# Kernel tuning notes

Hardware: AMD Instinct MI355X
Metric: run time of the kernel (lower is better)

Reference implementation:

```python
import jax, jax.numpy as jnp
import numpy as np

N = 100000
E = 1600000
D_IN = 128
D_OUT = 128


def setup_inputs() -> dict:
    key = jax.random.key(0)
    ks = jax.random.split(key, 6)
    seq = jax.random.normal(ks[0], (N, D_IN), dtype=jnp.float32)
    edge_src = jax.random.randint(ks[1], (E,), 0, N, dtype=jnp.int32)
    edge_dst = jax.random.randint(ks[2], (E,), 0, N, dtype=jnp.int32)
    adj_vals = jax.random.uniform(ks[3], (E,), dtype=jnp.float32)
    # xavier_uniform for [out, in] -> stored as [in, out] for x @ W
    lim = float(np.sqrt(6.0 / (D_IN + D_OUT)))
    w_fc = jax.random.uniform(ks[4], (D_IN, D_OUT), jnp.float32, -lim, lim)
    w_proj = jax.random.uniform(ks[5], (D_IN, D_OUT), jnp.float32, -lim, lim)
    b_proj = jnp.zeros((D_OUT,), jnp.float32)
    bias = jnp.zeros((D_OUT,), jnp.float32)
    return {"seq": seq, "edge_src": edge_src, "edge_dst": edge_dst,
            "adj_vals": adj_vals, "w_fc": w_fc, "w_proj": w_proj,
            "b_proj": b_proj, "bias": bias}


def reference(seq, edge_src, edge_dst, adj_vals, w_fc, w_proj, b_proj, bias):
    # h = fc(seq)  (no bias)
    h = seq @ w_fc                                  # [N, D_OUT]
    # spmm(adj, h): out[i] = sum_{e: dst=i} vals[e] * h[src[e]]
    msgs = adj_vals[:, None] * h[edge_src]          # [E, D_OUT]
    agg = jax.ops.segment_sum(msgs, edge_dst, num_segments=N)
    # bias add + residual proj(seq) add + tanh
    out = jnp.tanh(agg + bias + seq @ w_proj + b_proj)
    return out
```

## Files before the change

kernel.cpp:

```cpp
#include <hip/hip_runtime.h>
#include <math.h>


typedef __attribute__((ext_vector_type(8))) short short8;
typedef __attribute__((ext_vector_type(4))) float float4v;
typedef __attribute__((ext_vector_type(2))) _Float16 half2v;

#define PG 128
#define NBMAX 2048

static __device__ __forceinline__ short f2bf(float x) {
    unsigned u = __float_as_uint(x);
    unsigned r = (u + 0x7fffu + ((u >> 16) & 1u)) >> 16;
    return (short)r;
}
static __device__ __forceinline__ float bf2f(short h) {
    return __uint_as_float(((unsigned)(unsigned short)h) << 16);
}

__global__ __launch_bounds__(256)
void wconv_kernel(const float* __restrict__ w, short* __restrict__ whi,
                  short* __restrict__ wlo) {
    const int i = blockIdx.x * 256 + threadIdx.x;
    const float4 v = ((const float4*)w)[i];
    const int k = i >> 5;
    const int c4 = (i & 31) * 4;
    float xs[4] = {v.x, v.y, v.z, v.w};
    #pragma unroll
    for (int j = 0; j < 4; j++) {
        const short hi = f2bf(xs[j]);
        const short lo = f2bf(xs[j] - bf2f(hi));
        whi[(c4 + j) * 128 + k] = hi;
        wlo[(c4 + j) * 128 + k] = lo;
    }
}

#define KP 136

__global__ __launch_bounds__(256, 2)
void mm_mfma_kernel(const float* __restrict__ seq, const short* __restrict__ whi,
                    const short* __restrict__ wlo,
                    const float* __restrict__ b0p, const float* __restrict__ b1p,
                    float* __restrict__ out, _Float16* __restrict__ out16,
                    int N, int add_bias) {
    __shared__ short wt_hi[128 * KP];
    __shared__ short wt_lo[128 * KP];

    const int tid = threadIdx.x;
    for (int i = tid; i < 2048; i += 256) {
        const int row = i >> 4;
        const int k8  = (i & 15) * 8;
        *(float4*)&wt_hi[row * KP + k8] = ((const float4*)whi)[i];
        *(float4*)&wt_lo[row * KP + k8] = ((const float4*)wlo)[i];
    }
    __syncthreads();

    const int wave = tid >> 6;
    const int lane = tid & 63;
    const int q = lane >> 4;
    const int c = lane & 15;
    const int R = blockIdx.x * 64 + wave * 16;
    const int rowL = (R + c < N) ? (R + c) : (N - 1);

    float4v acc[8];
    #pragma unroll
    for (int ct = 0; ct < 8; ct++) acc[ct] = (float4v){0.f, 0.f, 0.f, 0.f};

    #pragma unroll
    for (int t = 0; t < 4; t++) {
        const int kk = t * 32 + q * 8;
        const float4 a0 = *(const float4*)&seq[(size_t)rowL * 128 + kk];
        const float4 a1 = *(const float4*)&seq[(size_t)rowL * 128 + kk + 4];
        float xs[8] = {a0.x, a0.y, a0.z, a0.w, a1.x, a1.y, a1.z, a1.w};
        union { short s[8]; short8 v; } ahi, alo;
        #pragma unroll
        for (int j = 0; j < 8; j++) {
            const short hi = f2bf(xs[j]);
            ahi.s[j] = hi;
            alo.s[j] = f2bf(xs[j] - bf2f(hi));
        }
        #pragma unroll
        for (int ct = 0; ct < 8; ct++) {
            const int n = ct * 16 + c;
            const short8 bhi = *(const short8*)&wt_hi[n * KP + kk];
            const short8 blo = *(const short8*)&wt_lo[n * KP + kk];
            acc[ct] = __builtin_amdgcn_mfma_f32_16x16x32_bf16(ahi.v, bhi, acc[ct], 0, 0, 0);
            acc[ct] = __builtin_amdgcn_mfma_f32_16x16x32_bf16(ahi.v, blo, acc[ct], 0, 0, 0);
            acc[ct] = __builtin_amdgcn_mfma_f32_16x16x32_bf16(alo.v, bhi, acc[ct], 0, 0, 0);
        }
    }

    if (out16) {
        #pragma unroll
        for (int ct = 0; ct < 8; ct++) {
            const int col = ct * 16 + c;
            #pragma unroll
            for (int r = 0; r < 4; r++) {
                const int row = R + q * 4 + r;
                if (row < N) out16[(size_t)row * 128 + col] = (_Float16)acc[ct][r];
            }
        }
    } else {
        #pragma unroll
        for (int ct = 0; ct < 8; ct++) {
            const int col = ct * 16 + c;
            float badd = 0.f;
            if (add_bias) badd = b0p[col] + b1p[col];
            #pragma unroll
            for (int r = 0; r < 4; r++) {
                const int row = R + q * 4 + r;
                if (row < N) out[(size_t)row * 128 + col] = acc[ct][r] + badd;
            }
        }
    }
}


__global__ __launch_bounds__(256)
void phist_kernel(const int* __restrict__ edst, int* __restrict__ hcnt,
                  int E, int S, int NB) {
    __shared__ int cnt[NBMAX];
    const int g = blockIdx.x;
    const int tid = threadIdx.x;
    for (int b = tid; b < NB; b += 256) cnt[b] = 0;
    __syncthreads();
    const int lo = g * S;
    const int hi = (lo + S < E) ? (lo + S) : E;
    for (int i = lo + tid; i < hi; i += 256)
        atomicAdd(&cnt[edst[i] >> 6], 1);
    __syncthreads();
    for (int b = tid; b < NB; b += 256) hcnt[b * PG + g] = cnt[b];
}

__global__ __launch_bounds__(256)
void pscan1_kernel(const int* __restrict__ in, int* __restrict__ out,
                   int* __restrict__ bsum, int L) {
    __shared__ int s[256];
    const int t = threadIdx.x;
    const int base = blockIdx.x * 1024 + t * 4;
    int v0 = (base + 0 < L) ? in[base + 0] : 0;
    int v1 = (base + 1 < L) ? in[base + 1] : 0;
    int v2 = (base + 2 < L) ? in[base + 2] : 0;
    int v3 = (base + 3 < L) ? in[base + 3] : 0;
    const int mysum = v0 + v1 + v2 + v3;
    s[t] = mysum;
    __syncthreads();
    for (int o = 1; o < 256; o <<= 1) {
        int add = (t >= o) ? s[t - o] : 0;
        __syncthreads();
        s[t] += add;
        __syncthreads();
    }
    const int excl = s[t] - mysum;
    if (base + 0 < L) out[base + 0] = excl;
    if (base + 1 < L) out[base + 1] = excl + v0;
    if (base + 2 < L) out[base + 2] = excl + v0 + v1;
    if (base + 3 < L) out[base + 3] = excl + v0 + v1 + v2;
    if (t == 255) bsum[blockIdx.x] = s[255];
}

__global__ __launch_bounds__(256)
void pscan2_kernel(const int* __restrict__ bsum, int* __restrict__ ebsum, int nb) {
    __shared__ int s[256];
    const int t = threadIdx.x;
    const int v = (t < nb) ? bsum[t] : 0;
    s[t] = v;
    __syncthreads();
    for (int o = 1; o < 256; o <<= 1) {
        int add = (t >= o) ? s[t - o] : 0;
        __syncthreads();
        s[t] += add;
        __syncthreads();
    }
    if (t < nb) ebsum[t] = s[t] - v;
}

__global__ __launch_bounds__(256)
void paddback_kernel(int* __restrict__ pos, const int* __restrict__ ebsum,
                     int* __restrict__ bstart, int L, int NB, int E) {
    const int add = ebsum[blockIdx.x];
    const int base = blockIdx.x * 1024 + threadIdx.x * 4;
    #pragma unroll
    for (int j = 0; j < 4; j++) {
        const int idx = base + j;
        if (idx < L) {
            const int v = pos[idx] + add;
            pos[idx] = v;
            if ((idx & (PG - 1)) == 0) bstart[idx / PG] = v;
        }
    }
    if (blockIdx.x == 0 && threadIdx.x == 0) bstart[NB] = E;
}

__global__ __launch_bounds__(256)
void pscatter_kernel(const int* __restrict__ esrc, const int* __restrict__ edst,
                     const float* __restrict__ vals, const int* __restrict__ pos,
                     int2* __restrict__ sedge, int E, int S, int NB) {
    __shared__ int cur[NBMAX];
    const int g = blockIdx.x;
    const int tid = threadIdx.x;
    for (int b = tid; b < NB; b += 256) cur[b] = pos[b * PG + g];
    __syncthreads();
    const int lo = g * S;
    const int hi = (lo + S < E) ? (lo + S) : E;
    for (int i = lo + tid; i < hi; i += 256) {
        const int d = edst[i];
        const int p = atomicAdd(&cur[d >> 6], 1);
        sedge[p] = make_int2((esrc[i] << 6) | (d & 63), __float_as_int(vals[i]));
    }
}

#define CAP 2048

__global__ __launch_bounds__(256, 8)
void aggregate_sorted(const int* __restrict__ bstart, const int2* __restrict__ sedge,
                      const _Float16* __restrict__ h, float* __restrict__ out, int N) {
    __shared__ int2 ebuf[CAP];
    __shared__ int cnt[64], sc[64], off[65], cur[64];
    const int b = blockIdx.x;
    const int tid = threadIdx.x;
    const int beg = bstart[b];
    const int total = bstart[b + 1] - beg;
    const int cl = total < CAP ? total : CAP;

    if (tid < 64) cnt[tid] = 0;
    __syncthreads();
    for (int i = tid; i < cl; i += 256)
        atomicAdd(&cnt[sedge[beg + i].x & 63], 1);
    __syncthreads();
    if (tid < 64) sc[tid] = cnt[tid];
    __syncthreads();
    for (int o = 1; o < 64; o <<= 1) {
        int add = (tid < 64 && tid >= o) ? sc[tid - o] : 0;
        __syncthreads();
        if (tid < 64) sc[tid] += add;
        __syncthreads();
    }
    if (tid < 64) { off[tid] = sc[tid] - cnt[tid]; cur[tid] = sc[tid] - cnt[tid]; }
    if (tid == 63) off[64] = sc[63];
    __syncthreads();
    for (int i = tid; i < cl; i += 256) {
        const int2 e = sedge[beg + i];
        const int p = atomicAdd(&cur[e.x & 63], 1);
        ebuf[p] = e;
    }
    __syncthreads();

    const int wave = tid >> 6;
    const int lane = tid & 63;
    const half2v* hp = (const half2v*)h;

    for (int n = wave * 16; n < wave * 16 + 16; n++) {
        const int node = b * 64 + n;
        if (node >= N) break;
        float2 acc = make_float2(0.f, 0.f);
        const int e0 = off[n], e1 = off[n + 1];
        int j = e0;
        for (; j + 4 <= e1; j += 4) {
            const int2 ea = ebuf[j], eb = ebuf[j + 1], ec = ebuf[j + 2], ed = ebuf[j + 3];
            const half2v h0 = hp[(size_t)(ea.x >> 6) * 64 + lane];
            const half2v h1 = hp[(size_t)(eb.x >> 6) * 64 + lane];
            const half2v h2 = hp[(size_t)(ec.x >> 6) * 64 + lane];
            const half2v h3 = hp[(size_t)(ed.x >> 6) * 64 + lane];
            const float v0 = __int_as_float(ea.y), v1 = __int_as_float(eb.y);
            const float v2 = __int_as_float(ec.y), v3 = __int_as_float(ed.y);
            acc.x += v0 * (float)h0.x; acc.y += v0 * (float)h0.y;
            acc.x += v1 * (float)h1.x; acc.y += v1 * (float)h1.y;
            acc.x += v2 * (float)h2.x; acc.y += v2 * (float)h2.y;
            acc.x += v3 * (float)h3.x; acc.y += v3 * (float)h3.y;
        }
        for (; j < e1; j++) {
            const int2 e = ebuf[j];
            const float v = __int_as_float(e.y);
            const half2v hv = hp[(size_t)(e.x >> 6) * 64 + lane];
            acc.x += v * (float)hv.x; acc.y += v * (float)hv.y;
        }
        for (int t2 = cl; t2 < total; t2++) {
            const int2 e = sedge[beg + t2];
            if ((e.x & 63) == n) {
                const float v = __int_as_float(e.y);
                const half2v hv = hp[(size_t)(e.x >> 6) * 64 + lane];
                acc.x += v * (float)hv.x; acc.y += v * (float)hv.y;
            }
        }
        union { double d; float2 f; } bv, rv;
        const double* op = (const double*)out + (size_t)node * 64 + lane;
        bv.d = __builtin_nontemporal_load(op);
        rv.f.x = tanhf(acc.x + bv.f.x);
        rv.f.y = tanhf(acc.y + bv.f.y);
        __builtin_nontemporal_store(rv.d, (double*)out + (size_t)node * 64 + lane);
    }
}


__global__ __launch_bounds__(256)
void edge_scatter(const int* __restrict__ esrc, const int* __restrict__ edst,
                  const float* __restrict__ vals, const _Float16* __restrict__ h,
                  float* __restrict__ out, int E) {
    const int gtid = blockIdx.x * blockDim.x + threadIdx.x;
    const int wave = gtid >> 6;
    const int lane = threadIdx.x & 63;
    const int nw = (gridDim.x * blockDim.x) >> 6;
    for (int e = wave; e < E; e += nw) {
        const int s = esrc[e];
        const int d = edst[e];
        const float v = vals[e];
        const half2v hv = *(const half2v*)(h + (size_t)s * 128 + lane * 2);
        float* op = out + (size_t)d * 128 + lane * 2;
        atomicAdd(op, v * (float)hv.x);
        atomicAdd(op + 1, v * (float)hv.y);
    }
}

__global__ __launch_bounds__(256)
void tanh_kernel(float* __restrict__ out, int n4) {
    const int i = blockIdx.x * blockDim.x + threadIdx.x;
    if (i < n4) {
        float4 v = ((float4*)out)[i];
        v.x = tanhf(v.x);
        v.y = tanhf(v.y);
        v.z = tanhf(v.z);
        v.w = tanhf(v.w);
        ((float4*)out)[i] = v;
    }
}

static inline size_t align64(size_t x) { return (x + 63) & ~(size_t)63; }

extern "C" void kernel_launch(void* const* d_in, const int* in_sizes, int n_in,
                              void* d_out, int out_size, void* d_ws, size_t ws_size,
                              hipStream_t stream) {
    const float* seq    = (const float*)d_in[0];
    const int*   esrc   = (const int*)  d_in[1];
    const int*   edst   = (const int*)  d_in[2];
    const float* vals   = (const float*)d_in[3];
    const float* w_fc   = (const float*)d_in[4];
    const float* w_proj = (const float*)d_in[5];
    const float* b_proj = (const float*)d_in[6];
    const float* bias   = (const float*)d_in[7];
    float* out = (float*)d_out;

    const int N = in_sizes[0] / 128;
    const int E = in_sizes[1];
    const int NB = (N + 63) >> 6;
    const int L  = NB * PG;
    const int S  = (E + PG - 1) / PG;
    const int nsb = (L + 1023) / 1024;

    char* ws = (char*)d_ws;
    const size_t o_h     = 0;
    const size_t o_whif  = align64(o_h    + (size_t)N * 128 * 2);
    const size_t o_wlof  = align64(o_whif + 32768);
    const size_t o_whip  = align64(o_wlof + 32768);
    const size_t o_wlop  = align64(o_whip + 32768);
    const size_t o_hc    = align64(o_wlop + 32768);
    const size_t o_pos   = align64(o_hc   + (size_t)L * 4);
    const size_t o_bs    = align64(o_pos  + (size_t)L * 4);
    const size_t o_bsum  = align64(o_bs   + (size_t)(NB + 1) * 4);
    const size_t o_ebs   = align64(o_bsum + 1024);
    const size_t o_sed   = align64(o_ebs  + 1024);
    const size_t need    = o_sed + (size_t)E * 8;

    _Float16* h   = (_Float16*)(ws + o_h);
    short* whi_fc = (short*)(ws + o_whif);
    short* wlo_fc = (short*)(ws + o_wlof);
    short* whi_pj = (short*)(ws + o_whip);
    short* wlo_pj = (short*)(ws + o_wlop);
    int*   hcnt   = (int*)  (ws + o_hc);
    int*   pos    = (int*)  (ws + o_pos);
    int*   bstart = (int*)  (ws + o_bs);
    int*   bsum   = (int*)  (ws + o_bsum);
    int*   ebsum  = (int*)  (ws + o_ebs);
    int2*  sedge  = (int2*) (ws + o_sed);

    const int mm_blocks = (N + 63) / 64;

    wconv_kernel<<<16, 256, 0, stream>>>(w_fc,   whi_fc, wlo_fc);
    wconv_kernel<<<16, 256, 0, stream>>>(w_proj, whi_pj, wlo_pj);
    mm_mfma_kernel<<<mm_blocks, 256, 0, stream>>>(seq, whi_fc, wlo_fc, nullptr, nullptr, nullptr, h, N, 0);
    mm_mfma_kernel<<<mm_blocks, 256, 0, stream>>>(seq, whi_pj, wlo_pj, b_proj, bias, out, nullptr, N, 1);

    if (ws_size >= need && NB <= NBMAX && nsb <= 256) {
        phist_kernel<<<PG, 256, 0, stream>>>(edst, hcnt, E, S, NB);
        pscan1_kernel<<<nsb, 256, 0, stream>>>(hcnt, pos, bsum, L);
        pscan2_kernel<<<1, 256, 0, stream>>>(bsum, ebsum, nsb);
        paddback_kernel<<<nsb, 256, 0, stream>>>(pos, ebsum, bstart, L, NB, E);
        pscatter_kernel<<<PG, 256, 0, stream>>>(esrc, edst, vals, pos, sedge, E, S, NB);
        aggregate_sorted<<<NB, 256, 0, stream>>>(bstart, sedge, h, out, N);
    } else {
        edge_scatter<<<8192, 256, 0, stream>>>(esrc, edst, vals, h, out, E);
        const int n4 = (N * 128) / 4;
        tanh_kernel<<<(n4 + 255) / 256, 256, 0, stream>>>(out, n4);
    }
}
```

Before: 348.7 us.

## Double partition groups, fuse weight conversion launches, unroll gather by eight

Raises the number of edge partition groups from 128 to 256 so the histogram and scatter passes spread across more blocks, and rescales the prefix-scan kernels to handle 2048 elements per block. The two weight-conversion launches become one 32-block launch. The aggregation gather loop gets an 8-way unrolled path and 32-bit byte-offset addressing to keep more loads in flight. In exchange the histogram table doubles in size and each block in the sorted aggregation runs more instructions.

After: 324.7 us. 6.9% less time.

```diff
diff --git a/kernel.cpp b/kernel.cpp
--- a/kernel.cpp
+++ b/kernel.cpp
@@ -6,7 +6,7 @@
 typedef __attribute__((ext_vector_type(4))) float float4v;
 typedef __attribute__((ext_vector_type(2))) _Float16 half2v;
 
-#define PG 128
+#define PG 256
 #define NBMAX 2048
 
 static __device__ __forceinline__ short f2bf(float x) {
@@ -19,9 +19,14 @@
 }
 
 __global__ __launch_bounds__(256)
-void wconv_kernel(const float* __restrict__ w, short* __restrict__ whi,
-                  short* __restrict__ wlo) {
-    const int i = blockIdx.x * 256 + threadIdx.x;
+void wconv_kernel(const float* __restrict__ wa, const float* __restrict__ wb,
+                  short* __restrict__ whia, short* __restrict__ wloa,
+                  short* __restrict__ whib, short* __restrict__ wlob) {
+    const int bb = blockIdx.x;
+    const float* w  = (bb < 16) ? wa   : wb;
+    short* whi      = (bb < 16) ? whia : whib;
+    short* wlo      = (bb < 16) ? wloa : wlob;
+    const int i = (bb & 15) * 256 + threadIdx.x;
     const float4 v = ((const float4*)w)[i];
     const int k = i >> 5;
     const int c4 = (i & 31) * 4;
@@ -137,12 +142,14 @@
                    int* __restrict__ bsum, int L) {
     __shared__ int s[256];
     const int t = threadIdx.x;
-    const int base = blockIdx.x * 1024 + t * 4;
-    int v0 = (base + 0 < L) ? in[base + 0] : 0;
-    int v1 = (base + 1 < L) ? in[base + 1] : 0;
-    int v2 = (base + 2 < L) ? in[base + 2] : 0;
-    int v3 = (base + 3 < L) ? in[base + 3] : 0;
-    const int mysum = v0 + v1 + v2 + v3;
+    const int base = blockIdx.x * 2048 + t * 8;
+    int v[8];
+    int mysum = 0;
+    #pragma unroll
+    for (int j = 0; j < 8; j++) {
+        v[j] = (base + j < L) ? in[base + j] : 0;
+        mysum += v[j];
+    }
     s[t] = mysum;
     __syncthreads();
     for (int o = 1; o < 256; o <<= 1) {
@@ -151,11 +158,12 @@
         s[t] += add;
         __syncthreads();
     }
-    const int excl = s[t] - mysum;
-    if (base + 0 < L) out[base + 0] = excl;
-    if (base + 1 < L) out[base + 1] = excl + v0;
-    if (base + 2 < L) out[base + 2] = excl + v0 + v1;
-    if (base + 3 < L) out[base + 3] = excl + v0 + v1 + v2;
+    int run = s[t] - mysum;
+    #pragma unroll
+    for (int j = 0; j < 8; j++) {
+        if (base + j < L) out[base + j] = run;
+        run += v[j];
+    }
     if (t == 255) bsum[blockIdx.x] = s[255];
 }
 
@@ -179,9 +187,9 @@
 void paddback_kernel(int* __restrict__ pos, const int* __restrict__ ebsum,
                      int* __restrict__ bstart, int L, int NB, int E) {
     const int add = ebsum[blockIdx.x];
-    const int base = blockIdx.x * 1024 + threadIdx.x * 4;
-    #pragma unroll
-    for (int j = 0; j < 4; j++) {
+    const int base = blockIdx.x * 2048 + threadIdx.x * 8;
+    #pragma unroll
+    for (int j = 0; j < 8; j++) {
         const int idx = base + j;
         if (idx < L) {
             const int v = pos[idx] + add;
@@ -248,7 +256,8 @@
 
     const int wave = tid >> 6;
     const int lane = tid & 63;
-    const half2v* hp = (const half2v*)h;
+    const char* hb = (const char*)h;
+    const int loff = lane << 2;
 
     for (int n = wave * 16; n < wave * 16 + 16; n++) {
         const int node = b * 64 + n;
@@ -256,12 +265,38 @@
         float2 acc = make_float2(0.f, 0.f);
         const int e0 = off[n], e1 = off[n + 1];
         int j = e0;
+        for (; j + 8 <= e1; j += 8) {
+            const int2 e0v = ebuf[j],     e1v = ebuf[j + 1];
+            const int2 e2v = ebuf[j + 2], e3v = ebuf[j + 3];
+            const int2 e4v = ebuf[j + 4], e5v = ebuf[j + 5];
+            const int2 e6v = ebuf[j + 6], e7v = ebuf[j + 7];
+            const half2v h0 = *(const half2v*)(hb + ((((unsigned)e0v.x >> 6) << 8) + loff));
+            const half2v h1 = *(const half2v*)(hb + ((((unsigned)e1v.x >> 6) << 8) + loff));
+            const half2v h2 = *(const half2v*)(hb + ((((unsigned)e2v.x >> 6) << 8) + loff));
+            const half2v h3 = *(const half2v*)(hb + ((((unsigned)e3v.x >> 6) << 8) + loff));
+            const half2v h4 = *(const half2v*)(hb + ((((unsigned)e4v.x >> 6) << 8) + loff));
+            const half2v h5 = *(const half2v*)(hb + ((((unsigned)e5v.x >> 6) << 8) + loff));
+            const half2v h6 = *(const half2v*)(hb + ((((unsigned)e6v.x >> 6) << 8) + loff));
+            const half2v h7 = *(const half2v*)(hb + ((((unsigned)e7v.x >> 6) << 8) + loff));
+            const float v0 = __int_as_float(e0v.y), v1 = __int_as_float(e1v.y);
+            const float v2 = __int_as_float(e2v.y), v3 = __int_as_float(e3v.y);
+            const float v4 = __int_as_float(e4v.y), v5 = __int_as_float(e5v.y);
+            const float v6 = __int_as_float(e6v.y), v7 = __int_as_float(e7v.y);
+            acc.x += v0 * (float)h0.x; acc.y += v0 * (float)h0.y;
+            acc.x += v1 * (float)h1.x; acc.y += v1 * (float)h1.y;
+            acc.x += v2 * (float)h2.x; acc.y += v2 * (float)h2.y;
+            acc.x += v3 * (float)h3.x; acc.y += v3 * (float)h3.y;
+            acc.x += v4 * (float)h4.x; acc.y += v4 * (float)h4.y;
+            acc.x += v5 * (float)h5.x; acc.y += v5 * (float)h5.y;
+            acc.x += v6 * (float)h6.x; acc.y += v6 * (float)h6.y;
+            acc.x += v7 * (float)h7.x; acc.y += v7 * (float)h7.y;
+        }
         for (; j + 4 <= e1; j += 4) {
             const int2 ea = ebuf[j], eb = ebuf[j + 1], ec = ebuf[j + 2], ed = ebuf[j + 3];
-            const half2v h0 = hp[(size_t)(ea.x >> 6) * 64 + lane];
-            const half2v h1 = hp[(size_t)(eb.x >> 6) * 64 + lane];
-            const half2v h2 = hp[(size_t)(ec.x >> 6) * 64 + lane];
-            const half2v h3 = hp[(size_t)(ed.x >> 6) * 64 + lane];
+            const half2v h0 = *(const half2v*)(hb + ((((unsigned)ea.x >> 6) << 8) + loff));
+            const half2v h1 = *(const half2v*)(hb + ((((unsigned)eb.x >> 6) << 8) + loff));
+            const half2v h2 = *(const half2v*)(hb + ((((unsigned)ec.x >> 6) << 8) + loff));
+            const half2v h3 = *(const half2v*)(hb + ((((unsigned)ed.x >> 6) << 8) + loff));
             const float v0 = __int_as_float(ea.y), v1 = __int_as_float(eb.y);
             const float v2 = __int_as_float(ec.y), v3 = __int_as_float(ed.y);
             acc.x += v0 * (float)h0.x; acc.y += v0 * (float)h0.y;
@@ -272,14 +307,14 @@
         for (; j < e1; j++) {
             const int2 e = ebuf[j];
             const float v = __int_as_float(e.y);
-            const half2v hv = hp[(size_t)(e.x >> 6) * 64 + lane];
+            const half2v hv = *(const half2v*)(hb + ((((unsigned)e.x >> 6) << 8) + loff));
             acc.x += v * (float)hv.x; acc.y += v * (float)hv.y;
         }
         for (int t2 = cl; t2 < total; t2++) {
             const int2 e = sedge[beg + t2];
             if ((e.x & 63) == n) {
                 const float v = __int_as_float(e.y);
-                const half2v hv = hp[(size_t)(e.x >> 6) * 64 + lane];
+                const half2v hv = *(const half2v*)(hb + ((((unsigned)e.x >> 6) << 8) + loff));
                 acc.x += v * (float)hv.x; acc.y += v * (float)hv.y;
             }
         }
@@ -345,7 +380,7 @@
     const int NB = (N + 63) >> 6;
     const int L  = NB * PG;
     const int S  = (E + PG - 1) / PG;
-    const int nsb = (L + 1023) / 1024;
+    const int nsb = (L + 2047) / 2048;
 
     char* ws = (char*)d_ws;
     const size_t o_h     = 0;
@@ -375,8 +410,7 @@
 
     const int mm_blocks = (N + 63) / 64;
 
-    wconv_kernel<<<16, 256, 0, stream>>>(w_fc,   whi_fc, wlo_fc);
-    wconv_kernel<<<16, 256, 0, stream>>>(w_proj, whi_pj, wlo_pj);
+    wconv_kernel<<<32, 256, 0, stream>>>(w_fc, w_proj, whi_fc, wlo_fc, whi_pj, wlo_pj);
     mm_mfma_kernel<<<mm_blocks, 256, 0, stream>>>(seq, whi_fc, wlo_fc, nullptr, nullptr, nullptr, h, N, 0);
     mm_mfma_kernel<<<mm_blocks, 256, 0, stream>>>(seq, whi_pj, wlo_pj, b_proj, bias, out, nullptr, N, 1);
 
```
